# Kernel optimization log

Measured on AMD Instinct MI355X. Metric: run time of the kernel, lower is better.

The kernel has to match this reference:

```python
import jax, jax.numpy as jnp
import numpy as np

H = 16   # num_heads
A = 64   # attn_size
D = 1024 # dims
NEG = -1000000000.0


def setup_inputs() -> dict:
    key = jax.random.key(0)
    k1, k2, k3, k4 = jax.random.split(key, 4)
    B, S = 2, 2048
    qs = jax.random.normal(k1, (B, S, D), dtype=jnp.float32)
    mask = jax.random.randint(k2, (B, S), 0, 2, dtype=jnp.int32)
    Wqkv = jax.random.normal(k3, (D, 3 * H * A), dtype=jnp.float32) * (1.0 / np.sqrt(D))
    Wout = jax.random.normal(k4, (H * A, D), dtype=jnp.float32) * (1.0 / np.sqrt(H * A))
    bout = jnp.zeros((D,), dtype=jnp.float32)
    return {"qs": qs, "mask": mask, "Wqkv": Wqkv, "Wout": Wout, "bout": bout}


def reference(qs, mask, Wqkv, Wout, bout):
    B, S, _ = qs.shape
    qkv = qs @ Wqkv                              # [B,S,3*H*A]
    qkv = qkv.reshape(B, S, 3 * H, A)            # split axis=2 in thirds (TF layout)
    q = jnp.transpose(qkv[:, :, 0:H, :], (0, 2, 1, 3))        # [B,H,S,A]
    k = jnp.transpose(qkv[:, :, H:2 * H, :], (0, 2, 1, 3))    # [B,H,S,A]
    v = jnp.transpose(qkv[:, :, 2 * H:3 * H, :], (0, 2, 1, 3))# [B,H,S,A]
    scores = jnp.einsum('bhqa,bhka->bhqk', q, k) / jnp.sqrt(jnp.float32(A))
    m = mask[:, None, None, :]                   # [B,1,1,S] broadcast over heads, queries
    scores = jnp.where(m == 0, NEG, scores)
    probs = jax.nn.softmax(scores, axis=-1)      # dropout_prob=0 / inference -> identity
    ctx = jnp.einsum('bhqk,bhka->bhqa', probs, v)  # [B,H,S,A]
    ctx = jnp.transpose(ctx, (0, 2, 1, 3)).reshape(B, S, H * A)
    return ctx @ Wout + bout
```

## Files before the change

kernel.cpp:

```cpp
#include <hip/hip_runtime.h>
#include <stdint.h>


typedef unsigned short u16;
typedef u16   u16x4  __attribute__((ext_vector_type(4)));
typedef u16   u16x8  __attribute__((ext_vector_type(8)));
typedef __bf16 bf16x8 __attribute__((ext_vector_type(8)));
typedef float f32x4  __attribute__((ext_vector_type(4)));

#define DEV __device__ __forceinline__

DEV u16 f2bf(float f) {
    uint32_t u = __builtin_bit_cast(uint32_t, f);
    u += 0x7fffu + ((u >> 16) & 1u);
    return (u16)(u >> 16);
}

DEV void async16(const void* g, void* l) {
    __builtin_amdgcn_global_load_lds(
        reinterpret_cast<const uint32_t __attribute__((address_space(1)))*>(
            reinterpret_cast<uintptr_t>(g)),
        reinterpret_cast<uint32_t __attribute__((address_space(3)))*>(
            reinterpret_cast<uintptr_t>(l)),
        16, 0, 0);
}

DEV f32x4 mfma16(bf16x8 a, bf16x8 b, f32x4 c) {
    return __builtin_amdgcn_mfma_f32_16x16x32_bf16(a, b, c, 0, 0, 0);
}


__global__ void k_conv(const float* __restrict__ src, u16* __restrict__ dst) {
    int i = (blockIdx.x * 256 + threadIdx.x) * 4;
    float4 v = *reinterpret_cast<const float4*>(src + i);
    u16x4 o = { f2bf(v.x), f2bf(v.y), f2bf(v.z), f2bf(v.w) };
    *reinterpret_cast<u16x4*>(dst + i) = o;
}

__global__ void k_tconv(const float* __restrict__ src, u16* __restrict__ dst, int R, int C) {
    __shared__ float t[32][33];
    int c0 = blockIdx.x * 32, r0 = blockIdx.y * 32;
    int tx = threadIdx.x, ty = threadIdx.y;
#pragma unroll
    for (int i = 0; i < 4; ++i)
        t[ty + 8 * i][tx] = src[(size_t)(r0 + ty + 8 * i) * C + c0 + tx];
    __syncthreads();
#pragma unroll
    for (int i = 0; i < 4; ++i)
        dst[(size_t)(c0 + ty + 8 * i) * R + r0 + tx] = f2bf(t[tx][ty + 8 * i]);
}

__global__ void k_mask(const int* __restrict__ m, float* __restrict__ b) {
    int i = blockIdx.x * 256 + threadIdx.x;
    b[i] = m[i] ? 0.0f : -1.0e9f;
}


template <bool OUT_BF16, bool HAS_BIAS>
__global__ __launch_bounds__(256, 2) void k_gemm(
    const u16* __restrict__ A, const u16* __restrict__ Bt,
    void* __restrict__ Cv, const float* __restrict__ bias,
    int M, int N, int K)
{
    __shared__ __attribute__((aligned(16))) u16 As[2][128 * 32];
    __shared__ __attribute__((aligned(16))) u16 Bs[2][128 * 32];

    const int tid = threadIdx.x, wave = tid >> 6, lane = tid & 63;
    const int lh = lane & 15, lg = lane >> 4;
    const int nbn = N >> 7;

    const int nwg = gridDim.x;
    const int q8 = nwg >> 3, r8 = nwg & 7;
    const int xcd = blockIdx.x & 7, li = blockIdx.x >> 3;
    const int wg = (xcd < r8 ? xcd * (q8 + 1) : r8 * (q8 + 1) + (xcd - r8) * q8) + li;

    const int m0 = (wg / nbn) * 128, n0 = (wg % nbn) * 128;
    const int wm = wave >> 1, wn = wave & 1;
    const int nk = K >> 5;

    auto stage = [&](int buf, int kt) {
#pragma unroll
        for (int i = 0; i < 2; ++i) {
            int c = (wave * 2 + i) * 64 + lane;
            int row = c >> 2, cc = c & 3;
            int sc = cc ^ (row & 3);
            async16(A  + (size_t)(m0 + row) * K + kt * 32 + sc * 8, &As[buf][(wave * 2 + i) * 512]);
            async16(Bt + (size_t)(n0 + row) * K + kt * 32 + sc * 8, &Bs[buf][(wave * 2 + i) * 512]);
        }
    };

    f32x4 acc[4][4] = {};
    stage(0, 0);
    for (int kt = 0; kt < nk; ++kt) {
        __syncthreads();
        if (kt + 1 < nk) stage((kt + 1) & 1, kt + 1);
        const int buf = kt & 1;
        bf16x8 af[4], bf_[4];
#pragma unroll
        for (int mt = 0; mt < 4; ++mt) {
            int row = wm * 64 + mt * 16 + lh;
            int off = row * 64 + ((lg * 16) ^ ((row & 3) << 4));
            af[mt] = __builtin_bit_cast(bf16x8,
                     *reinterpret_cast<const u16x8*>((const char*)&As[buf][0] + off));
        }
#pragma unroll
        for (int nt = 0; nt < 4; ++nt) {
            int row = wn * 64 + nt * 16 + lh;
            int off = row * 64 + ((lg * 16) ^ ((row & 3) << 4));
            bf_[nt] = __builtin_bit_cast(bf16x8,
                      *reinterpret_cast<const u16x8*>((const char*)&Bs[buf][0] + off));
        }
        __builtin_amdgcn_s_setprio(1);
#pragma unroll
        for (int mt = 0; mt < 4; ++mt)
#pragma unroll
            for (int nt = 0; nt < 4; ++nt)
                acc[mt][nt] = mfma16(af[mt], bf_[nt], acc[mt][nt]);
        __builtin_amdgcn_s_setprio(0);
        __syncthreads();
    }

#pragma unroll
    for (int mt = 0; mt < 4; ++mt)
#pragma unroll
        for (int nt = 0; nt < 4; ++nt) {
            int col = n0 + wn * 64 + nt * 16 + lh;
#pragma unroll
            for (int r = 0; r < 4; ++r) {
                int row = m0 + wm * 64 + mt * 16 + 4 * lg + r;
                float v = acc[mt][nt][r];
                if (HAS_BIAS) v += bias[col];
                if (OUT_BF16) ((u16*)Cv)[(size_t)row * N + col] = f2bf(v);
                else          ((float*)Cv)[(size_t)row * N + col] = v;
            }
        }
}


__global__ __launch_bounds__(512, 4) void k_attn(
    const u16* __restrict__ qkv, const float* __restrict__ biasg, u16* __restrict__ ctx)
{
    __shared__ __attribute__((aligned(16))) u16 Ks[2][64 * 64];
    __shared__ __attribute__((aligned(16))) u16 Vt[2][64 * 72];
    __shared__ __attribute__((aligned(16))) u16 Ps[8 * 16 * 72];

    const int tid = threadIdx.x, wave = tid >> 6, lane = tid & 63;
    const int lh = lane & 15, lg = lane >> 4;

    const int wg = (blockIdx.x & 7) * 64 + (blockIdx.x >> 3);
    const int qt = wg & 15, bh = wg >> 4;
    const int b = bh >> 4, h = bh & 15;

    const u16* qbase = qkv + ((size_t)b * 2048 * 48 + h) * 64;
    const u16* kbase = qkv + ((size_t)b * 2048 * 48 + 16 + h) * 64;
    const u16* vbase = qkv + ((size_t)b * 2048 * 48 + 32 + h) * 64;
    const float* brow = biasg + b * 2048;

    const int srow = wave * 8 + (lane >> 3);
    const int scc  = lane & 7;
    const int ksrc = scc ^ (srow & 7);
    const int vswz = srow ^ (scc << 3);

    bf16x8 qf[2];
    {
        int row = qt * 128 + wave * 16 + lh;
        qf[0] = __builtin_bit_cast(bf16x8,
            *reinterpret_cast<const u16x8*>(qbase + (size_t)row * 3072 + lg * 8));
        qf[1] = __builtin_bit_cast(bf16x8,
            *reinterpret_cast<const u16x8*>(qbase + (size_t)row * 3072 + 32 + lg * 8));
    }

    f32x4 oa[4] = {};
    float lst[4] = {0.0f, 0.0f, 0.0f, 0.0f};

    u16* Pw = &Ps[wave * 16 * 72];

    {
        async16(kbase + (size_t)srow * 3072 + ksrc * 8, &Ks[0][wave * 512]);
        u16x8 v = *reinterpret_cast<const u16x8*>(vbase + (size_t)srow * 3072 + scc * 8);
#pragma unroll
        for (int j = 0; j < 8; ++j) Vt[0][(scc * 8 + j) * 72 + vswz] = v[j];
    }

    for (int kt = 0; kt < 32; ++kt) {
        __syncthreads();
        const int buf = kt & 1;
        if (kt + 1 < 32) {
            async16(kbase + (size_t)((kt + 1) * 64 + srow) * 3072 + ksrc * 8, &Ks[buf ^ 1][wave * 512]);
            u16x8 v = *reinterpret_cast<const u16x8*>(
                vbase + (size_t)((kt + 1) * 64 + srow) * 3072 + scc * 8);
#pragma unroll
            for (int j = 0; j < 8; ++j) Vt[buf ^ 1][(scc * 8 + j) * 72 + vswz] = v[j];
        }

        float biasv[4];
#pragma unroll
        for (int nt = 0; nt < 4; ++nt) biasv[nt] = brow[kt * 64 + nt * 16 + lh];

        f32x4 sa[4] = {};
        __builtin_amdgcn_s_setprio(1);
#pragma unroll
        for (int ks = 0; ks < 2; ++ks) {
            bf16x8 kb[4];
#pragma unroll
            for (int nt = 0; nt < 4; ++nt) {
                int row = nt * 16 + lh;
                int off = row * 64 + (((ks * 4 + lg) ^ (row & 7)) << 3);
                kb[nt] = __builtin_bit_cast(bf16x8,
                         *reinterpret_cast<const u16x8*>(&Ks[buf][off]));
            }
#pragma unroll
            for (int nt = 0; nt < 4; ++nt)
                sa[nt] = mfma16(qf[ks], kb[nt], sa[nt]);
        }
        __builtin_amdgcn_s_setprio(0);

#pragma unroll
        for (int nt = 0; nt < 4; ++nt)
#pragma unroll
            for (int r = 0; r < 4; ++r) {
                float e = __expf(sa[nt][r] * 0.125f + biasv[nt]);
                lst[r] += e;
                Pw[(4 * lg + r) * 72 + nt * 16 + lh] = f2bf(e);
            }

        __builtin_amdgcn_s_setprio(1);
#pragma unroll
        for (int ks = 0; ks < 2; ++ks) {
            bf16x8 pa = __builtin_bit_cast(bf16x8,
                        *reinterpret_cast<const u16x8*>(Pw + lh * 72 + ks * 32 + lg * 8));
            bf16x8 vb[4];
#pragma unroll
            for (int nt = 0; nt < 4; ++nt) {
                int col = nt * 16 + lh;
                int g = (col >> 3) & 7;
                int off = col * 72 + (((ks * 4 + lg) ^ g) << 3);
                vb[nt] = __builtin_bit_cast(bf16x8,
                         *reinterpret_cast<const u16x8*>(&Vt[buf][off]));
            }
#pragma unroll
            for (int nt = 0; nt < 4; ++nt)
                oa[nt] = mfma16(pa, vb[nt], oa[nt]);
        }
        __builtin_amdgcn_s_setprio(0);
    }

#pragma unroll
    for (int r = 0; r < 4; ++r) {
        float s = lst[r];
#pragma unroll
        for (int o = 1; o < 16; o <<= 1) s += __shfl_xor(s, o);
        lst[r] = 1.0f / s;
    }

#pragma unroll
    for (int nt = 0; nt < 4; ++nt)
#pragma unroll
        for (int r = 0; r < 4; ++r) {
            int row = qt * 128 + wave * 16 + 4 * lg + r;
            ctx[(size_t)(b * 2048 + row) * 1024 + h * 64 + nt * 16 + lh] = f2bf(oa[nt][r] * lst[r]);
        }
}


extern "C" void kernel_launch(void* const* d_in, const int* in_sizes, int n_in,
                              void* d_out, int out_size, void* d_ws, size_t ws_size,
                              hipStream_t stream)
{
    const float* qs   = (const float*)d_in[0];
    const int*   mask = (const int*)d_in[1];
    const float* Wqkv = (const float*)d_in[2];
    const float* Wout = (const float*)d_in[3];
    const float* bout = (const float*)d_in[4];
    float* out = (float*)d_out;

    char* ws = (char*)d_ws;
    u16*   qs_bf = (u16*)(ws);
    u16*   WqkvT = (u16*)(ws + 8388608);
    u16*   WoutT = (u16*)(ws + 14680064);
    u16*   qkvb  = (u16*)(ws + 16777216);
    u16*   ctxb  = (u16*)(ws + 41943040);
    float* biasb = (float*)(ws + 50331648);

    k_conv<<<4096, 256, 0, stream>>>(qs, qs_bf);
    k_tconv<<<dim3(96, 32), dim3(32, 8), 0, stream>>>(Wqkv, WqkvT, 1024, 3072);
    k_tconv<<<dim3(32, 32), dim3(32, 8), 0, stream>>>(Wout, WoutT, 1024, 1024);
    k_mask<<<16, 256, 0, stream>>>(mask, biasb);

    k_gemm<true, false><<<768, 256, 0, stream>>>(qs_bf, WqkvT, qkvb, nullptr, 4096, 3072, 1024);
    k_attn<<<512, 512, 0, stream>>>(qkvb, biasb, ctxb);
    k_gemm<false, true><<<256, 256, 0, stream>>>(ctxb, WoutT, out, bout, 4096, 1024, 1024);
}
```

Baseline: 202.4 us.

## Keep softmax probabilities in registers via transposed QK^T and lane shuffles

```diff
diff --git a/kernel.cpp b/kernel.cpp
--- a/kernel.cpp
+++ b/kernel.cpp
@@ -3,17 +3,25 @@
 
 
 typedef unsigned short u16;
+typedef uint32_t u32;
 typedef u16   u16x4  __attribute__((ext_vector_type(4)));
 typedef u16   u16x8  __attribute__((ext_vector_type(8)));
+typedef u32   u32x4v __attribute__((ext_vector_type(4)));
 typedef __bf16 bf16x8 __attribute__((ext_vector_type(8)));
 typedef float f32x4  __attribute__((ext_vector_type(4)));
 
 #define DEV __device__ __forceinline__
 
 DEV u16 f2bf(float f) {
-    uint32_t u = __builtin_bit_cast(uint32_t, f);
+    u32 u = __builtin_bit_cast(u32, f);
     u += 0x7fffu + ((u >> 16) & 1u);
     return (u16)(u >> 16);
+}
+
+DEV u32 packbf(float a, float b) {
+    u16 x = __builtin_bit_cast(u16, (__bf16)a);
+    u16 y = __builtin_bit_cast(u16, (__bf16)b);
+    return (u32)x | ((u32)y << 16);
 }
 
 DEV void async16(const void* g, void* l) {
@@ -52,7 +60,7 @@
 
 __global__ void k_mask(const int* __restrict__ m, float* __restrict__ b) {
     int i = blockIdx.x * 256 + threadIdx.x;
-    b[i] = m[i] ? 0.0f : -1.0e9f;
+    b[i] = m[i] ? 0.0f : -1.442695e9f;
 }
 
 
@@ -142,10 +150,10 @@
 {
     __shared__ __attribute__((aligned(16))) u16 Ks[2][64 * 64];
     __shared__ __attribute__((aligned(16))) u16 Vt[2][64 * 72];
-    __shared__ __attribute__((aligned(16))) u16 Ps[8 * 16 * 72];
 
     const int tid = threadIdx.x, wave = tid >> 6, lane = tid & 63;
     const int lh = lane & 15, lg = lane >> 4;
+    const bool b5 = lg & 2, b4 = lg & 1;
 
     const int wg = (blockIdx.x & 7) * 64 + (blockIdx.x >> 3);
     const int qt = wg & 15, bh = wg >> 4;
@@ -171,9 +179,7 @@
     }
 
     f32x4 oa[4] = {};
-    float lst[4] = {0.0f, 0.0f, 0.0f, 0.0f};
-
-    u16* Pw = &Ps[wave * 16 * 72];
+    float lsum = 0.0f;
 
     {
         async16(kbase + (size_t)srow * 3072 + ksrc * 8, &Ks[0][wave * 512]);
@@ -193,9 +199,10 @@
             for (int j = 0; j < 8; ++j) Vt[buf ^ 1][(scc * 8 + j) * 72 + vswz] = v[j];
         }
 
-        float biasv[4];
-#pragma unroll
-        for (int nt = 0; nt < 4; ++nt) biasv[nt] = brow[kt * 64 + nt * 16 + lh];
+        float4 bias4[4];
+#pragma unroll
+        for (int nt = 0; nt < 4; ++nt)
+            bias4[nt] = *reinterpret_cast<const float4*>(brow + kt * 64 + nt * 16 + 4 * lg);
 
         f32x4 sa[4] = {};
         __builtin_amdgcn_s_setprio(1);
@@ -211,24 +218,58 @@
             }
 #pragma unroll
             for (int nt = 0; nt < 4; ++nt)
-                sa[nt] = mfma16(qf[ks], kb[nt], sa[nt]);
+                sa[nt] = mfma16(kb[nt], qf[ks], sa[nt]);
         }
         __builtin_amdgcn_s_setprio(0);
 
-#pragma unroll
-        for (int nt = 0; nt < 4; ++nt)
-#pragma unroll
-            for (int r = 0; r < 4; ++r) {
-                float e = __expf(sa[nt][r] * 0.125f + biasv[nt]);
-                lst[r] += e;
-                Pw[(4 * lg + r) * 72 + nt * 16 + lh] = f2bf(e);
-            }
+        const float SC = 0.1803368801111244f;
+        u32 U[4][2];
+#pragma unroll
+        for (int nt = 0; nt < 4; ++nt) {
+            float e0 = __builtin_exp2f(fmaf(sa[nt][0], SC, bias4[nt].x));
+            float e1 = __builtin_exp2f(fmaf(sa[nt][1], SC, bias4[nt].y));
+            float e2 = __builtin_exp2f(fmaf(sa[nt][2], SC, bias4[nt].z));
+            float e3 = __builtin_exp2f(fmaf(sa[nt][3], SC, bias4[nt].w));
+            lsum += (e0 + e1) + (e2 + e3);
+            U[nt][0] = packbf(e0, e1);
+            U[nt][1] = packbf(e2, e3);
+        }
+
+        u32 V1[2][2][2], F[2][2][2];
+        {
+            u32 S1[2][2], Y[2][2];
+#pragma unroll
+            for (int n1 = 0; n1 < 2; ++n1)
+#pragma unroll
+                for (int hh = 0; hh < 2; ++hh) {
+                    S1[n1][hh] = b5 ? U[2 * n1][hh] : U[2 * n1 + 1][hh];
+                    Y[n1][hh] = (u32)__shfl_xor((int)S1[n1][hh], 32);
+                    u32 kp = b5 ? U[2 * n1 + 1][hh] : U[2 * n1][hh];
+                    V1[0][n1][hh] = b5 ? Y[n1][hh] : kp;
+                    V1[1][n1][hh] = b5 ? kp : Y[n1][hh];
+                }
+            u32 S2[2][2], Z[2][2];
+#pragma unroll
+            for (int n1 = 0; n1 < 2; ++n1)
+#pragma unroll
+                for (int hh = 0; hh < 2; ++hh) {
+                    S2[n1][hh] = b4 ? V1[0][n1][hh] : V1[1][n1][hh];
+                    Z[n1][hh] = (u32)__shfl_xor((int)S2[n1][hh], 16);
+                    u32 kp = b4 ? V1[1][n1][hh] : V1[0][n1][hh];
+                    F[0][n1][hh] = b4 ? Z[n1][hh] : kp;
+                    F[1][n1][hh] = b4 ? kp : Z[n1][hh];
+                }
+        }
+        bf16x8 pa[2];
+#pragma unroll
+        for (int ks = 0; ks < 2; ++ks) {
+            u32x4v w = { F[0][ks][0], F[0][ks][1], F[1][ks][0], F[1][ks][1] };
+            pa[ks] = __builtin_bit_cast(bf16x8, w);
+        }
 
         __builtin_amdgcn_s_setprio(1);
 #pragma unroll
         for (int ks = 0; ks < 2; ++ks) {
-            bf16x8 pa = __builtin_bit_cast(bf16x8,
-                        *reinterpret_cast<const u16x8*>(Pw + lh * 72 + ks * 32 + lg * 8));
             bf16x8 vb[4];
 #pragma unroll
             for (int nt = 0; nt < 4; ++nt) {
@@ -240,25 +281,27 @@
             }
 #pragma unroll
             for (int nt = 0; nt < 4; ++nt)
-                oa[nt] = mfma16(pa, vb[nt], oa[nt]);
+                oa[nt] = mfma16(pa[ks], vb[nt], oa[nt]);
         }
         __builtin_amdgcn_s_setprio(0);
     }
 
-#pragma unroll
-    for (int r = 0; r < 4; ++r) {
-        float s = lst[r];
-#pragma unroll
-        for (int o = 1; o < 16; o <<= 1) s += __shfl_xor(s, o);
-        lst[r] = 1.0f / s;
-    }
+    float s = lsum;
+    s += __shfl_xor(s, 16);
+    s += __shfl_xor(s, 32);
+    float inv = 1.0f / s;
+
+    float invq[4];
+#pragma unroll
+    for (int r = 0; r < 4; ++r)
+        invq[r] = __shfl(inv, 4 * lg + r);
 
 #pragma unroll
     for (int nt = 0; nt < 4; ++nt)
 #pragma unroll
         for (int r = 0; r < 4; ++r) {
             int row = qt * 128 + wave * 16 + 4 * lg + r;
-            ctx[(size_t)(b * 2048 + row) * 1024 + h * 64 + nt * 16 + lh] = f2bf(oa[nt][r] * lst[r]);
+            ctx[(size_t)(b * 2048 + row) * 1024 + h * 64 + nt * 16 + lh] = f2bf(oa[nt][r] * invq[r]);
         }
 }
 
```

After: 214.5 us. 1.06x slower.
